# Kernel tuning notes

Hardware: AMD Instinct MI355X
Metric: run time of the kernel (lower is better)

The kernel has to match this reference:

```python
import jax, jax.numpy as jnp
import numpy as np

B, S, D, H, DIL = 4, 4096, 768, 12, 8
HD = D // H  # head dim = 64


def setup_inputs() -> dict:
    key = jax.random.key(0)
    ks = jax.random.split(key, 9)
    def w(k):
        return jax.random.normal(k, (D, D), jnp.float32) * 0.02
    def b(k):
        return jax.random.normal(k, (D,), jnp.float32) * 0.02
    return {
        "x": jax.random.normal(ks[0], (B, S, D), jnp.float32),
        "Wq": w(ks[1]), "bq": b(ks[2]),
        "Wk": w(ks[3]), "bk": b(ks[4]),
        "Wv": w(ks[5]), "bv": b(ks[6]),
        "Wo": w(ks[7]), "bo": b(ks[8]),
    }


def reference(x, Wq, bq, Wk, bk, Wv, bv, Wo, bo):
    Bs, Sl, _ = x.shape
    # torch.nn.Linear: y = x @ W.T + b
    q = (x @ Wq.T + bq).reshape(Bs, Sl, H, HD).transpose(0, 2, 1, 3)  # [B,H,S,hd]
    k = (x @ Wk.T + bk).reshape(Bs, Sl, H, HD).transpose(0, 2, 1, 3)
    v = (x @ Wv.T + bv).reshape(Bs, Sl, H, HD).transpose(0, 2, 1, 3)
    # Since S % DIL == 0, the per-position index set
    #   arange(max(0, i - DIL*(S//DIL)), min(S, i + DIL*(S//DIL)+1), DIL)
    # equals arange(0, S, DIL) for every i -> one batched gather + attention.
    idx = jnp.arange(0, Sl, DIL)
    k_d = k[:, :, idx, :]  # [B,H,S/DIL,hd]
    v_d = v[:, :, idx, :]
    scale = 1.0 / np.sqrt(HD).astype(np.float32)
    scores = jnp.einsum('bhqd,bhkd->bhqk', q, k_d) * scale  # [B,H,S,S/DIL]
    attn = jax.nn.softmax(scores, axis=-1)  # dropout: eval mode, identity
    ctx = jnp.einsum('bhqk,bhkd->bhqd', attn, v_d)  # [B,H,S,hd]
    ctx = ctx.transpose(0, 2, 1, 3).reshape(Bs, Sl, D)
    return ctx @ Wo.T + bo
```

## Files before the change

### kernel.cpp

```cpp
#include <hip/hip_runtime.h>

typedef __attribute__((ext_vector_type(8))) short short8;
typedef __attribute__((ext_vector_type(4))) short short4v;
typedef __attribute__((ext_vector_type(4))) float f32x4;
typedef __attribute__((ext_vector_type(4))) unsigned uint32x4;

#define AS1 __attribute__((address_space(1)))
#define AS3 __attribute__((address_space(3)))

__device__ __forceinline__ void gld16(const void* g, void* l) {
  __builtin_amdgcn_global_load_lds((const AS1 void*)g, (AS3 void*)l, 16, 0, 0);
}

__device__ __forceinline__ short f2bf(float f) {
  unsigned u = __builtin_bit_cast(unsigned, f);
  unsigned r = (u + 0x7fffu + ((u >> 16) & 1u)) >> 16;
  return (short)r;
}

template <int N>
__device__ __forceinline__ void wait_vm() {
  asm volatile("s_waitcnt vmcnt(%0)" ::"i"(N) : "memory");
}
__device__ __forceinline__ void bar() { __builtin_amdgcn_s_barrier(); }

#define MFMA(a, b, c) __builtin_amdgcn_mfma_f32_16x16x32_bf16((a), (b), (c), 0, 0, 0)

__global__ void cast_f32_bf16(const float* __restrict__ in, short* __restrict__ out, int n4) {
  int i = blockIdx.x * 256 + threadIdx.x;
  if (i >= n4) return;
  f32x4 v = ((const f32x4*)in)[i];
  short4v o;
  o[0] = f2bf(v[0]); o[1] = f2bf(v[1]); o[2] = f2bf(v[2]); o[3] = f2bf(v[3]);
  ((short4v*)out)[i] = o;
}

__global__ void cast4_f32_bf16(const float* __restrict__ s0, const float* __restrict__ s1,
                               const float* __restrict__ s2, const float* __restrict__ s3,
                               short* __restrict__ out) {
  const float* src = (blockIdx.y == 0) ? s0 : (blockIdx.y == 1) ? s1 : (blockIdx.y == 2) ? s2 : s3;
  int i = blockIdx.x * 256 + threadIdx.x;
  f32x4 v = ((const f32x4*)src)[i];
  short4v o;
  o[0] = f2bf(v[0]); o[1] = f2bf(v[1]); o[2] = f2bf(v[2]); o[3] = f2bf(v[3]);
  ((short4v*)(out + (size_t)blockIdx.y * 589824))[i] = o;
}

template <int OUT>
__global__ __launch_bounds__(256) void gemm_bt(const short* __restrict__ A, int lda,
                                               const short* __restrict__ B,
                                               const float* __restrict__ bias,
                                               const float* __restrict__ bias2,
                                               void* __restrict__ Cv, void* __restrict__ Cv2,
                                               int K, float oscale) {
  __shared__ alignas(16) short As[128 * 64];
  __shared__ alignas(16) short Bs[128 * 64];
  const int tid = threadIdx.x, wave = tid >> 6, lane = tid & 63;
  const int bm = blockIdx.x * 128, bn = blockIdx.y * 128;
  const int wr = (wave >> 1) * 64, wc = (wave & 1) * 64;
  const int l15 = lane & 15, g = lane >> 4;
  const int srow = lane >> 3;
  const int sb = ((lane & 7) * 16) ^ (srow << 4);
  const int rswz = (l15 & 7) << 4;

  f32x4 zero = {0.f, 0.f, 0.f, 0.f};
  f32x4 acc[4][4];
#pragma unroll
  for (int m = 0; m < 4; ++m)
#pragma unroll
    for (int n = 0; n < 4; ++n) acc[m][n] = zero;

  for (int kt = 0; kt < K; kt += 64) {
#pragma unroll
    for (int c = 0; c < 4; ++c) {
      int chunk = wave * 4 + c;
      int r = chunk * 8 + srow;
      gld16(A + (size_t)(bm + r) * lda + kt + (sb >> 1), (char*)As + chunk * 1024);
      gld16(B + (size_t)(bn + r) * 768 + kt + (sb >> 1), (char*)Bs + chunk * 1024);
    }
    __syncthreads();
#pragma unroll
    for (int kk = 0; kk < 2; ++kk) {
      short8 af[4], bfr[4];
#pragma unroll
      for (int m = 0; m < 4; ++m)
        af[m] = *(const short8*)((const char*)As + (wr + 16 * m + l15) * 128 +
                                 ((kk * 64 + g * 16) ^ rswz));
#pragma unroll
      for (int n = 0; n < 4; ++n)
        bfr[n] = *(const short8*)((const char*)Bs + (wc + 16 * n + l15) * 128 +
                                  ((kk * 64 + g * 16) ^ rswz));
#pragma unroll
      for (int m = 0; m < 4; ++m)
#pragma unroll
        for (int n = 0; n < 4; ++n) acc[m][n] = MFMA(af[m], bfr[n], acc[m][n]);
    }
    __syncthreads();
  }

#pragma unroll
  for (int m = 0; m < 4; ++m)
#pragma unroll
    for (int n = 0; n < 4; ++n) {
      int col = bn + wc + 16 * n + l15;
      if (OUT == 3 && col >= 768) {
        float bv = bias2[col - 768];
        int hh = col - 768;
        int h = hh >> 6, d = hh & 63;
        int row0 = bm + wr + 16 * m + g * 4;
        int bb = row0 >> 9, kloc = row0 & 511;
        int slot = ((kloc >> 5) << 5) + (((kloc >> 2) & 3) << 3) + (((kloc >> 4) & 1) << 2);
        short4v pk;
#pragma unroll
        for (int r = 0; r < 4; ++r) pk[r] = f2bf((acc[m][n][r] + bv) * oscale);
        *(short4v*)((short*)Cv2 + (size_t)((bb * 12 + h) * 64 + d) * 512 + slot) = pk;
      } else {
        float bv = bias[col];
#pragma unroll
        for (int r = 0; r < 4; ++r) {
          int row = bm + wr + 16 * m + g * 4 + r;
          float v = (acc[m][n][r] + bv) * oscale;
          if (OUT == 0)
            ((float*)Cv)[(size_t)row * 768 + col] = v;
          else
            ((short*)Cv)[(size_t)row * 768 + col] = f2bf(v);
        }
      }
    }
}

__global__ __launch_bounds__(256, 2) void attn_kernel(const short* __restrict__ qb,
                                                      const short* __restrict__ kb,
                                                      const short* __restrict__ vt,
                                                      short* __restrict__ ctxb) {
  __shared__ alignas(16) char lds[32768];
  char* bufA = lds;
  char* bufB = lds + 16384;
  const int tid = threadIdx.x, wave = tid >> 6, lane = tid & 63;
  const int b = blockIdx.y / 12, h = blockIdx.y % 12;
  const int qbase = blockIdx.x * 64;
  const int l15 = lane & 15, g = lane >> 4, g4 = g * 4;

  const short* qrow = qb + (size_t)(b * 4096 + qbase + wave * 16 + l15) * 768 + h * 64 + g * 8;
  short8 qa0 = *(const short8*)(qrow);
  short8 qa1 = *(const short8*)(qrow + 32);

  f32x4 zero = {0.f, 0.f, 0.f, 0.f};
  f32x4 st[32];

  const int krow_g = (lane & 7) * 16;
  const int kkey = wave * 32 + (lane >> 3);
  const int vd = wave * 16 + (lane >> 4);
  const int vcol = (lane & 15) * 16;
  const size_t kgbase = (size_t)(b * 512) * 768 + h * 64;
  const size_t vgbase = (size_t)((b * 12 + h) * 64) * 512;
  const int kswz = (l15 & 7) << 4;

#define STAGE_K(ci, dst)                                                              \
  _Pragma("unroll") for (int c = 0; c < 4; ++c) {                                     \
    int key = kkey + c * 8;                                                           \
    int sb = krow_g ^ ((key & 7) << 4);                                               \
    gld16(kb + kgbase + (size_t)((ci)*128 + key) * 768 + (sb >> 1),                   \
          (dst) + (wave * 32 + c * 8) * 128);                                         \
  }
#define STAGE_V(ci, dst)                                                              \
  _Pragma("unroll") for (int c = 0; c < 4; ++c) {                                     \
    int d = vd + c * 4;                                                               \
    int sb = vcol ^ ((d & 7) << 4);                                                   \
    gld16(vt + vgbase + (size_t)d * 512 + (ci)*128 + (sb >> 1),                       \
          (dst) + (wave * 16 + c * 4) * 256);                                         \
  }
#define QK_CHUNK(ci, buf)                                                             \
  __builtin_amdgcn_s_setprio(1);                                                      \
  _Pragma("unroll") for (int t = 0; t < 8; ++t) {                                     \
    int base = (t * 16 + l15) * 128;                                                  \
    short8 k0 = *(const short8*)((buf) + (base + ((g * 16) ^ kswz)));                 \
    short8 k1 = *(const short8*)((buf) + (base + ((g * 16 + 64) ^ kswz)));            \
    f32x4 a = MFMA(k0, qa0, zero);                                                    \
    st[(ci)*8 + t] = MFMA(k1, qa1, a);                                                \
  }                                                                                   \
  __builtin_amdgcn_s_setprio(0);
#define PV_CHUNK(ci, buf)                                                             \
  __builtin_amdgcn_s_setprio(1);                                                      \
  _Pragma("unroll") for (int kk = 0; kk < 4; ++kk) {                                  \
    f32x4 s0 = st[(ci)*8 + 2 * kk], s1 = st[(ci)*8 + 2 * kk + 1];                     \
    uint32x4 u;                                                                       \
    asm("v_cvt_pk_bf16_f32 %0, %1, %2" : "=v"(u[0]) : "v"(s0[0]), "v"(s0[1]));        \
    asm("v_cvt_pk_bf16_f32 %0, %1, %2" : "=v"(u[1]) : "v"(s0[2]), "v"(s0[3]));        \
    asm("v_cvt_pk_bf16_f32 %0, %1, %2" : "=v"(u[2]) : "v"(s1[0]), "v"(s1[1]));        \
    asm("v_cvt_pk_bf16_f32 %0, %1, %2" : "=v"(u[3]) : "v"(s1[2]), "v"(s1[3]));        \
    short8 pa = __builtin_bit_cast(short8, u);                                        \
    _Pragma("unroll") for (int n = 0; n < 4; ++n) {                                   \
      int row = 16 * n + l15;                                                         \
      short8 vf = *(const short8*)((buf) + row * 256 + ((kk * 64 + g * 16) ^ ((row & 7) << 4))); \
      ctx[n] = MFMA(pa, vf, ctx[n]);                                                  \
    }                                                                                 \
  }                                                                                   \
  __builtin_amdgcn_s_setprio(0);

  STAGE_K(0, bufA);
  STAGE_K(1, bufB);

  wait_vm<4>(); bar();
  QK_CHUNK(0, bufA);
  bar(); asm volatile("" ::: "memory");
  STAGE_K(2, bufA);

  wait_vm<4>(); bar();
  QK_CHUNK(1, bufB);
  bar(); asm volatile("" ::: "memory");
  STAGE_K(3, bufB);

  wait_vm<4>(); bar();
  QK_CHUNK(2, bufA);
  bar(); asm volatile("" ::: "memory");
  STAGE_V(0, bufA);

  wait_vm<4>(); bar();
  QK_CHUNK(3, bufB);
  bar(); asm volatile("" ::: "memory");
  STAGE_V(1, bufB);

  float m = st[0][0];
#pragma unroll
  for (int t = 0; t < 32; ++t)
#pragma unroll
    for (int r = 0; r < 4; ++r) m = fmaxf(m, st[t][r]);
  m = fmaxf(m, __shfl_xor(m, 16, 64));
  m = fmaxf(m, __shfl_xor(m, 32, 64));
  float l = 0.f;
#pragma unroll
  for (int t = 0; t < 32; ++t)
#pragma unroll
    for (int r = 0; r < 4; ++r) {
      float p = __builtin_amdgcn_exp2f(st[t][r] - m);
      st[t][r] = p;
      l += p;
    }
  l += __shfl_xor(l, 16, 64);
  l += __shfl_xor(l, 32, 64);

  f32x4 ctx[4];
#pragma unroll
  for (int n = 0; n < 4; ++n) ctx[n] = zero;

  wait_vm<4>(); bar();
  PV_CHUNK(0, bufA);
  bar(); asm volatile("" ::: "memory");
  STAGE_V(2, bufA);

  wait_vm<4>(); bar();
  PV_CHUNK(1, bufB);
  bar(); asm volatile("" ::: "memory");
  STAGE_V(3, bufB);

  wait_vm<4>(); bar();
  PV_CHUNK(2, bufA);

  wait_vm<0>(); bar();
  PV_CHUNK(3, bufB);

  float rinv = 1.0f / l;
  float rw0 = __shfl(rinv, g4, 64), rw1 = __shfl(rinv, g4 + 1, 64);
  float rw2 = __shfl(rinv, g4 + 2, 64), rw3 = __shfl(rinv, g4 + 3, 64);
  size_t rowbase = (size_t)(b * 4096 + qbase + wave * 16);
#pragma unroll
  for (int n = 0; n < 4; ++n) {
    int col = h * 64 + 16 * n + l15;
    ctxb[(rowbase + g4 + 0) * 768 + col] = f2bf(ctx[n][0] * rw0);
    ctxb[(rowbase + g4 + 1) * 768 + col] = f2bf(ctx[n][1] * rw1);
    ctxb[(rowbase + g4 + 2) * 768 + col] = f2bf(ctx[n][2] * rw2);
    ctxb[(rowbase + g4 + 3) * 768 + col] = f2bf(ctx[n][3] * rw3);
  }
#undef STAGE_K
#undef STAGE_V
#undef QK_CHUNK
#undef PV_CHUNK
}

extern "C" void kernel_launch(void* const* d_in, const int* in_sizes, int n_in,
                              void* d_out, int out_size, void* d_ws, size_t ws_size,
                              hipStream_t stream) {
  const float* x  = (const float*)d_in[0];
  const float* Wq = (const float*)d_in[1];
  const float* bq = (const float*)d_in[2];
  const float* Wk = (const float*)d_in[3];
  const float* bk = (const float*)d_in[4];
  const float* Wv = (const float*)d_in[5];
  const float* bv = (const float*)d_in[6];
  const float* Wo = (const float*)d_in[7];
  const float* bo = (const float*)d_in[8];

  char* ws = (char*)d_ws;
  const size_t XB_OFF = 0;
  const size_t WQ_OFF = 25165824;
  const size_t WK_OFF = WQ_OFF + 1179648;
  const size_t WV_OFF = WK_OFF + 1179648;
  const size_t WO_OFF = WV_OFF + 1179648;
  const size_t Q_OFF  = WO_OFF + 1179648;
  const size_t K_OFF  = Q_OFF + 25165824;
  const size_t V_OFF  = K_OFF + 3145728;

  short* xb   = (short*)(ws + XB_OFF);
  short* ctxb = xb;
  short* wqb  = (short*)(ws + WQ_OFF);
  short* wkb  = (short*)(ws + WK_OFF);
  short* wob  = (short*)(ws + WO_OFF);
  short* qbf  = (short*)(ws + Q_OFF);
  short* kbf  = (short*)(ws + K_OFF);
  short* vtb  = (short*)(ws + V_OFF);

  cast_f32_bf16<<<12288, 256, 0, stream>>>(x, xb, 3145728);
  cast4_f32_bf16<<<dim3(576, 4), 256, 0, stream>>>(Wq, Wk, Wv, Wo, wqb);

  const float QSCALE = 0.18033688011112042f;

  gemm_bt<1><<<dim3(128, 6), 256, 0, stream>>>(xb, 768, wqb, bq, nullptr, qbf, nullptr, 768, QSCALE);
  gemm_bt<3><<<dim3(16, 12), 256, 0, stream>>>(xb, 6144, wkb, bk, bv, kbf, vtb, 768, 1.0f);

  attn_kernel<<<dim3(64, 48), 256, 0, stream>>>(qbf, kbf, vtb, ctxb);

  gemm_bt<0><<<dim3(128, 6), 256, 0, stream>>>(ctxb, 768, wob, bo, nullptr, d_out, nullptr, 768, 1.0f);
}
```

Baseline: 236.9 us.

## Use 256x256 double-buffered GEMM tiles with 512-thread blocks for projections

Replaces the 128x128 single-buffered projection GEMM with a 256x256 tile kernel using 8 waves, 128KB LDS split into two stages, and prefetch of the next K-tile while computing the current one. It aims to raise operand reuse per LDS load and to overlap global loads with MFMA work, and it raises wave priority during the compute phase. The trade-off is far fewer blocks (192 or 48), which may underfill the GPU's CUs, and much higher LDS and register pressure. The 2-blocks-per-CU launch bound cannot be met with 128KB of LDS per block.

```diff
diff --git a/kernel.cpp b/kernel.cpp
--- a/kernel.cpp
+++ b/kernel.cpp
@@ -47,59 +47,71 @@
 }
 
 template <int OUT>
-__global__ __launch_bounds__(256) void gemm_bt(const short* __restrict__ A, int lda,
-                                               const short* __restrict__ B,
-                                               const float* __restrict__ bias,
-                                               const float* __restrict__ bias2,
-                                               void* __restrict__ Cv, void* __restrict__ Cv2,
-                                               int K, float oscale) {
-  __shared__ alignas(16) short As[128 * 64];
-  __shared__ alignas(16) short Bs[128 * 64];
+__global__ __launch_bounds__(512, 2) void gemm256(const short* __restrict__ A, int lda,
+                                                  const short* __restrict__ B,
+                                                  const float* __restrict__ bias,
+                                                  const float* __restrict__ bias2,
+                                                  void* __restrict__ Cv, void* __restrict__ Cv2,
+                                                  int K, float oscale) {
+  __shared__ alignas(16) char lds[131072];
   const int tid = threadIdx.x, wave = tid >> 6, lane = tid & 63;
-  const int bm = blockIdx.x * 128, bn = blockIdx.y * 128;
-  const int wr = (wave >> 1) * 64, wc = (wave & 1) * 64;
-  const int l15 = lane & 15, g = lane >> 4;
-  const int srow = lane >> 3;
-  const int sb = ((lane & 7) * 16) ^ (srow << 4);
+  const int bm = blockIdx.x * 256, bn = blockIdx.y * 256;
+  const int wr = (wave >> 2) * 128, wc = (wave & 3) * 64;
+  const int l15 = lane & 15, g = lane >> 4, g4 = g * 4;
+  const int srow8 = lane >> 3;
+  const int sb = ((lane & 7) * 16) ^ (srow8 << 4);
   const int rswz = (l15 & 7) << 4;
 
-  f32x4 zero = {0.f, 0.f, 0.f, 0.f};
-  f32x4 acc[4][4];
-#pragma unroll
-  for (int m = 0; m < 4; ++m)
-#pragma unroll
-    for (int n = 0; n < 4; ++n) acc[m][n] = zero;
-
-  for (int kt = 0; kt < K; kt += 64) {
-#pragma unroll
-    for (int c = 0; c < 4; ++c) {
-      int chunk = wave * 4 + c;
-      int r = chunk * 8 + srow;
-      gld16(A + (size_t)(bm + r) * lda + kt + (sb >> 1), (char*)As + chunk * 1024);
-      gld16(B + (size_t)(bn + r) * 768 + kt + (sb >> 1), (char*)Bs + chunk * 1024);
+  f32x4 acc[8][4];
+#pragma unroll
+  for (int m = 0; m < 8; ++m)
+#pragma unroll
+    for (int n = 0; n < 4; ++n) acc[m][n] = f32x4{0.f, 0.f, 0.f, 0.f};
+
+#define GSTAGE(t, d)                                                                  \
+  { int kt = (t) << 6;                                                                \
+    _Pragma("unroll") for (int c = 0; c < 4; ++c) {                                   \
+      int rr = c * 64 + wave * 8;                                                     \
+      gld16(A + (size_t)(bm + rr + srow8) * lda + kt + (sb >> 1),                     \
+            lds + (d) * 65536 + rr * 128);                                            \
+      gld16(B + (size_t)(bn + rr + srow8) * 768 + kt + (sb >> 1),                     \
+            lds + (d) * 65536 + 32768 + rr * 128);                                    \
+    } }
+
+  const int nt = K >> 6;
+  GSTAGE(0, 0);
+
+  for (int t = 0; t < nt; ++t) {
+    const int cb = t & 1;
+    bar();
+    asm volatile("" ::: "memory");
+    if (t + 1 < nt) { GSTAGE(t + 1, cb ^ 1); }
+    if (t + 1 < nt) { wait_vm<8>(); } else { wait_vm<0>(); }
+    bar();
+    asm volatile("" ::: "memory");
+
+    const char* Ab = lds + cb * 65536;
+    const char* Bb = Ab + 32768;
+    __builtin_amdgcn_s_setprio(1);
+#pragma unroll
+    for (int kk = 0; kk < 2; ++kk) {
+      short8 bfr[4];
+#pragma unroll
+      for (int n = 0; n < 4; ++n)
+        bfr[n] = *(const short8*)(Bb + (wc + 16 * n + l15) * 128 + ((kk * 64 + g * 16) ^ rswz));
+#pragma unroll
+      for (int m = 0; m < 8; ++m) {
+        short8 af = *(const short8*)(Ab + (wr + 16 * m + l15) * 128 + ((kk * 64 + g * 16) ^ rswz));
+#pragma unroll
+        for (int n = 0; n < 4; ++n) acc[m][n] = MFMA(af, bfr[n], acc[m][n]);
+      }
     }
-    __syncthreads();
-#pragma unroll
-    for (int kk = 0; kk < 2; ++kk) {
-      short8 af[4], bfr[4];
-#pragma unroll
-      for (int m = 0; m < 4; ++m)
-        af[m] = *(const short8*)((const char*)As + (wr + 16 * m + l15) * 128 +
-                                 ((kk * 64 + g * 16) ^ rswz));
-#pragma unroll
-      for (int n = 0; n < 4; ++n)
-        bfr[n] = *(const short8*)((const char*)Bs + (wc + 16 * n + l15) * 128 +
-                                  ((kk * 64 + g * 16) ^ rswz));
-#pragma unroll
-      for (int m = 0; m < 4; ++m)
-#pragma unroll
-        for (int n = 0; n < 4; ++n) acc[m][n] = MFMA(af[m], bfr[n], acc[m][n]);
-    }
-    __syncthreads();
+    __builtin_amdgcn_s_setprio(0);
   }
-
-#pragma unroll
-  for (int m = 0; m < 4; ++m)
+#undef GSTAGE
+
+#pragma unroll
+  for (int m = 0; m < 8; ++m)
 #pragma unroll
     for (int n = 0; n < 4; ++n) {
       int col = bn + wc + 16 * n + l15;
@@ -107,7 +119,7 @@
         float bv = bias2[col - 768];
         int hh = col - 768;
         int h = hh >> 6, d = hh & 63;
-        int row0 = bm + wr + 16 * m + g * 4;
+        int row0 = bm + wr + 16 * m + g4;
         int bb = row0 >> 9, kloc = row0 & 511;
         int slot = ((kloc >> 5) << 5) + (((kloc >> 2) & 3) << 3) + (((kloc >> 4) & 1) << 2);
         short4v pk;
@@ -118,7 +130,7 @@
         float bv = bias[col];
 #pragma unroll
         for (int r = 0; r < 4; ++r) {
-          int row = bm + wr + 16 * m + g * 4 + r;
+          int row = bm + wr + 16 * m + g4 + r;
           float v = (acc[m][n][r] + bv) * oscale;
           if (OUT == 0)
             ((float*)Cv)[(size_t)row * 768 + col] = v;
@@ -315,10 +327,10 @@
 
   const float QSCALE = 0.18033688011112042f;
 
-  gemm_bt<1><<<dim3(128, 6), 256, 0, stream>>>(xb, 768, wqb, bq, nullptr, qbf, nullptr, 768, QSCALE);
-  gemm_bt<3><<<dim3(16, 12), 256, 0, stream>>>(xb, 6144, wkb, bk, bv, kbf, vtb, 768, 1.0f);
+  gemm256<1><<<dim3(64, 3), 512, 0, stream>>>(xb, 768, wqb, bq, nullptr, qbf, nullptr, 768, QSCALE);
+  gemm256<3><<<dim3(8, 6), 512, 0, stream>>>(xb, 6144, wkb, bk, bv, kbf, vtb, 768, 1.0f);
 
   attn_kernel<<<dim3(64, 48), 256, 0, stream>>>(qbf, kbf, vtb, ctxb);
 
-  gemm_bt<0><<<dim3(128, 6), 256, 0, stream>>>(ctxb, 768, wob, bo, nullptr, d_out, nullptr, 768, 1.0f);
-}
+  gemm256<0><<<dim3(64, 3), 512, 0, stream>>>(ctxb, 768, wob, bo, nullptr, d_out, nullptr, 768, 1.0f);
+}
```

Result: slower. 251.9 us (+6.3%).
